# Optimization experiments

Hardware: AMD Instinct MI355X
Metric: run time of the kernel (lower is better)

Reference implementation:

```python
import jax, jax.numpy as jnp
import numpy as np

KLD_SCALE = 10.0
COMMITMENT_COST = 0.1


def setup_inputs() -> dict:
    key = jax.random.key(0)
    k1, k2 = jax.random.split(key)
    z = jax.random.normal(k1, (32, 2048, 64), dtype=jnp.float32)
    codebook = jax.random.normal(k2, (1024, 64), dtype=jnp.float32)
    return {"z": z, "codebook": codebook}


def reference(z, codebook):
    B, N, D = z.shape
    z_e = z.reshape(B * N, D)                          # (M, D)
    # squared euclidean distance: ||z||^2 - 2 z.E^T + ||E||^2
    dist = (
        jnp.sum(z_e * z_e, axis=1, keepdims=True)
        - 2.0 * (z_e @ codebook.T)
        + jnp.sum(codebook * codebook, axis=1)[None, :]
    )                                                  # (M, K)
    ind = jnp.argmin(dist, axis=1)                     # (M,)
    z_q = codebook[ind]                                # (M, D) gather
    latent_loss = (
        COMMITMENT_COST * jnp.mean((jax.lax.stop_gradient(z_q) - z_e) ** 2)
        + jnp.mean((z_q - jax.lax.stop_gradient(z_e)) ** 2)
    ) * KLD_SCALE
    # straight-through estimator
    z_q_st = z_e + jax.lax.stop_gradient(z_q - z_e)
    return z_q_st.reshape(B, N, D), latent_loss
```

## Files before the change

kernel.cpp:

```cpp
#include <hip/hip_runtime.h>
#include <hip/hip_bf16.h>
#include <float.h>

#define DIMS 64
#define KC 1024
#define M_TOTAL 65536
#define TAU 4e-3f

typedef __attribute__((ext_vector_type(8))) short bf16x8;
typedef __attribute__((ext_vector_type(4))) float f32x4;

#define SE_OFF   0
#define CTL_OFF  1024
#define PART_OFF 2048
#define PBH_OFF  4096
#define PBL_OFF  36864
#define IDX_OFF  69632
#define WL_OFF   135168

__device__ inline short f2bf(float x) {
  union { __hip_bfloat16 h; short s; } u;
  u.h = __float2bfloat16(x);
  return u.s;
}
__device__ inline float bf2f(short x) {
  union { short s; __hip_bfloat16 h; } u;
  u.s = x;
  return __bfloat162float(u.h);
}

__device__ inline void gload_lds16(const void* g, void* l) {
  __builtin_amdgcn_global_load_lds(
      (const __attribute__((address_space(1))) void*)g,
      (__attribute__((address_space(3))) void*)l, 16, 0, 0);
}

__global__ __launch_bounds__(256) void k_prep(const float* __restrict__ cb,
                                              float* __restrict__ se,
                                              unsigned int* __restrict__ ctl,
                                              unsigned short* __restrict__ pbh,
                                              unsigned short* __restrict__ pbl) {
  const int tid = blockIdx.x * 256 + threadIdx.x;
  if (tid < 4) ctl[tid] = 0;
  const int l = tid & 63;
  const int s = (tid >> 6) & 1;
  const int tt = tid >> 7;
  const int code = tt * 16 + (l & 15);
  const int k = s * 32 + (l >> 4) * 8;
  const float* p = cb + (size_t)code * DIMS + k;
  float v[8];
  ((float4*)v)[0] = ((const float4*)p)[0];
  ((float4*)v)[1] = ((const float4*)p)[1];
  bf16x8 h, lo;
#pragma unroll
  for (int j = 0; j < 8; ++j) {
    short hj = f2bf(v[j]);
    h[j] = hj;
    lo[j] = f2bf(v[j] - bf2f(hj));
  }
  *(bf16x8*)(pbh + (size_t)tid * 8) = h;
  *(bf16x8*)(pbl + (size_t)tid * 8) = lo;

  if (tid < KC) {
    const float4* q = (const float4*)(cb + (size_t)tid * DIMS);
    float a0 = 0.f, a1 = 0.f, a2 = 0.f, a3 = 0.f;
#pragma unroll
    for (int i = 0; i < DIMS / 4; ++i) {
      float4 u = q[i];
      a0 = fmaf(u.x, u.x, a0);
      a1 = fmaf(u.y, u.y, a1);
      a2 = fmaf(u.z, u.z, a2);
      a3 = fmaf(u.w, u.w, a3);
    }
    se[tid] = (a0 + a1) + (a2 + a3);
  }
}

__global__ __launch_bounds__(256, 4) void k_dist(const float* __restrict__ z,
                                                 const unsigned short* __restrict__ pbh,
                                                 const unsigned short* __restrict__ pbl,
                                                 const float* __restrict__ se,
                                                 int* __restrict__ idxo,
                                                 int* __restrict__ wl,
                                                 unsigned int* __restrict__ ctl) {
  __shared__ bf16x8 sB[2][2][256];
  const int l = threadIdx.x & 63;
  const int w = threadIdx.x >> 6;
  const int r0 = blockIdx.x * 64 + w * 16;
  const int col = l & 15;
  const int g = l >> 4;

  bf16x8 ah[2], al[2];
  {
    const float* zp = z + (size_t)(r0 + col) * DIMS + g * 8;
#pragma unroll
    for (int ks = 0; ks < 2; ++ks) {
      float v[8];
      ((float4*)v)[0] = ((const float4*)(zp + ks * 32))[0];
      ((float4*)v)[1] = ((const float4*)(zp + ks * 32))[1];
#pragma unroll
      for (int j = 0; j < 8; ++j) {
        short hj = f2bf(v[j]);
        ah[ks][j] = hj;
        al[ks][j] = f2bf(v[j] - bf2f(hj));
      }
    }
  }

  float m1[4] = {FLT_MAX, FLT_MAX, FLT_MAX, FLT_MAX};
  float m2[4] = {FLT_MAX, FLT_MAX, FLT_MAX, FLT_MAX};
  int bt[4] = {0, 0, 0, 0};

  {
    const int f = w * 64 + l;
    gload_lds16(pbh + (size_t)f * 8, &sB[0][0][w * 64]);
    gload_lds16(pbl + (size_t)f * 8, &sB[0][1][w * 64]);
  }
  __syncthreads();

  int cur = 0;
  for (int c = 0; c < 32; ++c) {
    if (c + 1 < 32) {
      const size_t f = (size_t)(c + 1) * 256 + w * 64 + l;
      gload_lds16(pbh + f * 8, &sB[cur ^ 1][0][w * 64]);
      gload_lds16(pbl + f * 8, &sB[cur ^ 1][1][w * 64]);
    }
#pragma unroll
    for (int tt = 0; tt < 2; ++tt) {
      const int t = c * 2 + tt;
      bf16x8 bh0 = sB[cur][0][tt * 128 + l];
      bf16x8 bh1 = sB[cur][0][tt * 128 + 64 + l];
      bf16x8 bl0 = sB[cur][1][tt * 128 + l];
      bf16x8 bl1 = sB[cur][1][tt * 128 + 64 + l];
      const float sec = se[t * 16 + col];
      f32x4 acc = {0.f, 0.f, 0.f, 0.f};
      acc = __builtin_amdgcn_mfma_f32_16x16x32_bf16(ah[0], bh0, acc, 0, 0, 0);
      acc = __builtin_amdgcn_mfma_f32_16x16x32_bf16(ah[1], bh1, acc, 0, 0, 0);
      acc = __builtin_amdgcn_mfma_f32_16x16x32_bf16(ah[0], bl0, acc, 0, 0, 0);
      acc = __builtin_amdgcn_mfma_f32_16x16x32_bf16(ah[1], bl1, acc, 0, 0, 0);
      acc = __builtin_amdgcn_mfma_f32_16x16x32_bf16(al[0], bh0, acc, 0, 0, 0);
      acc = __builtin_amdgcn_mfma_f32_16x16x32_bf16(al[1], bh1, acc, 0, 0, 0);
#pragma unroll
      for (int j = 0; j < 4; ++j) {
        float d = fmaf(-2.f, acc[j], sec);
        float nm2 = __builtin_amdgcn_fmed3f(d, m1[j], m2[j]);
        bool lt = d < m1[j];
        m1[j] = lt ? d : m1[j];
        bt[j] = lt ? t : bt[j];
        m2[j] = nm2;
      }
    }
    __syncthreads();
    cur ^= 1;
  }

#pragma unroll
  for (int j = 0; j < 4; ++j) {
    float m1j = m1[j], m2j = m2[j];
    int ij = bt[j] * 16 + col;
    for (int msk = 1; msk <= 8; msk <<= 1) {
      float o1 = __shfl_xor(m1j, msk);
      float o2 = __shfl_xor(m2j, msk);
      int oi = __shfl_xor(ij, msk);
      bool take = (o1 < m1j) || (o1 == m1j && oi < ij);
      float hi = take ? m1j : o1;
      m2j = fminf(fminf(m2j, o2), hi);
      m1j = take ? o1 : m1j;
      ij = take ? oi : ij;
    }
    if (col == 0) {
      const int row = r0 + g * 4 + j;
      idxo[row] = ij;
      if (m2j - m1j < TAU) {
        int p = atomicAdd((int*)ctl, 1);
        wl[p] = row;
      }
    }
  }
}

__global__ __launch_bounds__(256) void k_refine(const float* __restrict__ z,
                                                const float* __restrict__ cb,
                                                const int* __restrict__ wl,
                                                const unsigned int* __restrict__ ctl,
                                                int* __restrict__ idxo) {
  __shared__ float zz[64];
  __shared__ double sd[256];
  __shared__ int si[256];
  const int t = threadIdx.x;
  const int n = (int)ctl[0];
  for (int wi = blockIdx.x; wi < n; wi += 1024) {
    const int row = wl[wi];
    if (t < 16) ((float4*)zz)[t] = ((const float4*)(z + (size_t)row * DIMS))[t];
    __syncthreads();
    const int c0 = t * 4;
    double accd[4] = {0.0, 0.0, 0.0, 0.0};
    for (int ch = 0; ch < 4; ++ch) {
      float zr[16];
#pragma unroll
      for (int q = 0; q < 4; ++q) ((float4*)zr)[q] = ((float4*)zz)[ch * 4 + q];
#pragma unroll
      for (int cc = 0; cc < 4; ++cc) {
        const float* e = cb + (size_t)(c0 + cc) * DIMS + ch * 16;
#pragma unroll
        for (int q = 0; q < 16; ++q) {
          double df = (double)zr[q] - (double)e[q];
          accd[cc] = fma(df, df, accd[cc]);
        }
      }
    }
    double best = 1e300;
    int bi = 0;
#pragma unroll
    for (int cc = 0; cc < 4; ++cc)
      if (accd[cc] < best) { best = accd[cc]; bi = c0 + cc; }
    sd[t] = best;
    si[t] = bi;
    __syncthreads();
    for (int off = 128; off > 0; off >>= 1) {
      if (t < off) {
        double ob = sd[t + off];
        int oi = si[t + off];
        if (ob < sd[t] || (ob == sd[t] && oi < si[t])) { sd[t] = ob; si[t] = oi; }
      }
      __syncthreads();
    }
    if (t == 0) idxo[row] = si[0];
    __syncthreads();
  }
}

__global__ __launch_bounds__(256) void k_out(const float* __restrict__ z,
                                             const float* __restrict__ cb,
                                             const int* __restrict__ idxi,
                                             float* __restrict__ out,
                                             float* __restrict__ partials) {
  const int tid = blockIdx.x * 256 + threadIdx.x;
  const int row = tid >> 2;
  const int q = tid & 3;
  const int code = idxi[row];
  const float4* zp = (const float4*)(z + (size_t)row * DIMS + q * 16);
  const float4* ep = (const float4*)(cb + (size_t)code * DIMS + q * 16);
  float4* op = (float4*)(out + (size_t)row * DIMS + q * 16);
  float sse = 0.f;
#pragma unroll
  for (int i = 0; i < 4; ++i) {
    float4 v = zp[i], e = ep[i];
    float dx = e.x - v.x, dy = e.y - v.y, dz = e.z - v.z, dw = e.w - v.w;
    sse = fmaf(dx, dx, sse);
    sse = fmaf(dy, dy, sse);
    sse = fmaf(dz, dz, sse);
    sse = fmaf(dw, dw, sse);
    float4 o;
    o.x = v.x + dx;
    o.y = v.y + dy;
    o.z = v.z + dz;
    o.w = v.w + dw;
    op[i] = o;
  }
  __shared__ float sh[256];
  sh[threadIdx.x] = sse;
  __syncthreads();
  for (int off = 128; off > 0; off >>= 1) {
    if (threadIdx.x < off) sh[threadIdx.x] += sh[threadIdx.x + off];
    __syncthreads();
  }
  if (threadIdx.x == 0) partials[blockIdx.x] = sh[0];
}

__global__ __launch_bounds__(256) void k_loss(const float* __restrict__ partials,
                                              float* __restrict__ out) {
  __shared__ float sh[256];
  const int t = threadIdx.x;
  sh[t] = partials[t] + partials[t + 256] + partials[t + 512] + partials[t + 768];
  __syncthreads();
  for (int off = 128; off > 0; off >>= 1) {
    if (t < off) sh[t] += sh[t + off];
    __syncthreads();
  }
  if (t == 0) {
    out[(size_t)M_TOTAL * DIMS] = sh[0] * (11.0f / (float)((size_t)M_TOTAL * DIMS));
  }
}

extern "C" void kernel_launch(void* const* d_in, const int* in_sizes, int n_in,
                              void* d_out, int out_size, void* d_ws, size_t ws_size,
                              hipStream_t stream) {
  const float* z = (const float*)d_in[0];
  const float* cb = (const float*)d_in[1];
  float* out = (float*)d_out;
  float* ws = (float*)d_ws;

  float* se = ws + SE_OFF;
  unsigned int* ctl = (unsigned int*)(ws + CTL_OFF);
  float* partials = ws + PART_OFF;
  unsigned short* pbh = (unsigned short*)(ws + PBH_OFF);
  unsigned short* pbl = (unsigned short*)(ws + PBL_OFF);
  int* idx = (int*)(ws + IDX_OFF);
  int* wl = (int*)(ws + WL_OFF);

  k_prep<<<32, 256, 0, stream>>>(cb, se, ctl, pbh, pbl);
  k_dist<<<M_TOTAL / 64, 256, 0, stream>>>(z, pbh, pbl, se, idx, wl, ctl);
  k_refine<<<1024, 256, 0, stream>>>(z, cb, wl, ctl, idx);
  k_out<<<M_TOTAL / 64, 256, 0, stream>>>(z, cb, idx, out, partials);
  k_loss<<<1, 256, 0, stream>>>(partials, out);
}
```

Measured before the change: 61.39 us.

## Split codebook scan across two blocks per row tile and merge top-2 results

The distance kernel now splits the 1024-entry codebook into two halves, so each row tile is handled by two blocks that each scan 512 codes, doubling grid size. It also raises the launch-bounds occupancy hint to 8 blocks. Per-half best/second-best distances and indices go to workspace, and a new merge kernel combines them and builds the ambiguous-row worklist. This targets low occupancy or parallelism in k_dist, at the cost of recomputing the z bf16 split per half, extra global traffic, and another kernel launch.

```diff
diff --git a/kernel.cpp b/kernel.cpp
--- a/kernel.cpp
+++ b/kernel.cpp
@@ -15,8 +15,10 @@
 #define PART_OFF 2048
 #define PBH_OFF  4096
 #define PBL_OFF  36864
-#define IDX_OFF  69632
-#define WL_OFF   135168
+#define M1_OFF   69632
+#define M2_OFF   200704
+#define IDX_OFF  331776
+#define WL_OFF   462848
 
 __device__ inline short f2bf(float x) {
   union { __hip_bfloat16 h; short s; } u;
@@ -76,17 +78,19 @@
   }
 }
 
-__global__ __launch_bounds__(256, 4) void k_dist(const float* __restrict__ z,
+__global__ __launch_bounds__(256, 8) void k_dist(const float* __restrict__ z,
                                                  const unsigned short* __restrict__ pbh,
                                                  const unsigned short* __restrict__ pbl,
                                                  const float* __restrict__ se,
-                                                 int* __restrict__ idxo,
-                                                 int* __restrict__ wl,
-                                                 unsigned int* __restrict__ ctl) {
+                                                 float* __restrict__ m1o,
+                                                 float* __restrict__ m2o,
+                                                 int* __restrict__ idxo) {
   __shared__ bf16x8 sB[2][2][256];
   const int l = threadIdx.x & 63;
   const int w = threadIdx.x >> 6;
-  const int r0 = blockIdx.x * 64 + w * 16;
+  const int split = blockIdx.x & 1;
+  const int rb = blockIdx.x >> 1;
+  const int r0 = rb * 64 + w * 16;
   const int col = l & 15;
   const int g = l >> 4;
 
@@ -111,23 +115,24 @@
   float m2[4] = {FLT_MAX, FLT_MAX, FLT_MAX, FLT_MAX};
   int bt[4] = {0, 0, 0, 0};
 
+  const int C0 = split * 16;
   {
-    const int f = w * 64 + l;
-    gload_lds16(pbh + (size_t)f * 8, &sB[0][0][w * 64]);
-    gload_lds16(pbl + (size_t)f * 8, &sB[0][1][w * 64]);
+    const size_t f = (size_t)C0 * 256 + w * 64 + l;
+    gload_lds16(pbh + f * 8, &sB[0][0][w * 64]);
+    gload_lds16(pbl + f * 8, &sB[0][1][w * 64]);
   }
   __syncthreads();
 
   int cur = 0;
-  for (int c = 0; c < 32; ++c) {
-    if (c + 1 < 32) {
-      const size_t f = (size_t)(c + 1) * 256 + w * 64 + l;
+  for (int c = 0; c < 16; ++c) {
+    if (c + 1 < 16) {
+      const size_t f = (size_t)(C0 + c + 1) * 256 + w * 64 + l;
       gload_lds16(pbh + f * 8, &sB[cur ^ 1][0][w * 64]);
       gload_lds16(pbl + f * 8, &sB[cur ^ 1][1][w * 64]);
     }
 #pragma unroll
     for (int tt = 0; tt < 2; ++tt) {
-      const int t = c * 2 + tt;
+      const int t = (C0 + c) * 2 + tt;
       bf16x8 bh0 = sB[cur][0][tt * 128 + l];
       bf16x8 bh1 = sB[cur][0][tt * 128 + 64 + l];
       bf16x8 bl0 = sB[cur][1][tt * 128 + l];
@@ -169,13 +174,29 @@
       ij = take ? oi : ij;
     }
     if (col == 0) {
-      const int row = r0 + g * 4 + j;
-      idxo[row] = ij;
-      if (m2j - m1j < TAU) {
-        int p = atomicAdd((int*)ctl, 1);
-        wl[p] = row;
-      }
-    }
+      const int o = split * M_TOTAL + r0 + g * 4 + j;
+      m1o[o] = m1j;
+      m2o[o] = m2j;
+      idxo[o] = ij;
+    }
+  }
+}
+
+__global__ __launch_bounds__(256) void k_merge(const float* __restrict__ m1s,
+                                               const float* __restrict__ m2s,
+                                               int* __restrict__ idxs,
+                                               int* __restrict__ wl,
+                                               unsigned int* __restrict__ ctl) {
+  const int row = blockIdx.x * 256 + threadIdx.x;
+  const float a1 = m1s[row], b1 = m1s[M_TOTAL + row];
+  const float a2 = m2s[row], b2 = m2s[M_TOTAL + row];
+  const int ia = idxs[row], ib = idxs[M_TOTAL + row];
+  const float m1 = fminf(a1, b1);
+  const float m2 = fminf(fmaxf(a1, b1), fminf(a2, b2));
+  idxs[row] = (b1 < a1) ? ib : ia;
+  if (m2 - m1 < TAU) {
+    int p = atomicAdd((int*)ctl, 1);
+    wl[p] = row;
   }
 }
 
@@ -296,11 +317,14 @@
   float* partials = ws + PART_OFF;
   unsigned short* pbh = (unsigned short*)(ws + PBH_OFF);
   unsigned short* pbl = (unsigned short*)(ws + PBL_OFF);
+  float* m1s = ws + M1_OFF;
+  float* m2s = ws + M2_OFF;
   int* idx = (int*)(ws + IDX_OFF);
   int* wl = (int*)(ws + WL_OFF);
 
   k_prep<<<32, 256, 0, stream>>>(cb, se, ctl, pbh, pbl);
-  k_dist<<<M_TOTAL / 64, 256, 0, stream>>>(z, pbh, pbl, se, idx, wl, ctl);
+  k_dist<<<(M_TOTAL / 64) * 2, 256, 0, stream>>>(z, pbh, pbl, se, m1s, m2s, idx);
+  k_merge<<<M_TOTAL / 256, 256, 0, stream>>>(m1s, m2s, idx, wl, ctl);
   k_refine<<<1024, 256, 0, stream>>>(z, cb, wl, ctl, idx);
   k_out<<<M_TOTAL / 64, 256, 0, stream>>>(z, cb, idx, out, partials);
   k_loss<<<1, 256, 0, stream>>>(partials, out);
```

New measurement: 80.81 us. 1.32x slower.

## Fuse output gather and per-row SSE into distance kernel, refine patches rows

Applied to the files above, without the earlier changes.

Moves the output gather, straight-through write and squared-error computation into the distance kernel's epilogue, using the block's argmin indices held in shared memory. Per-row SSE values go to a workspace array. The refine kernel now rewrites the output row and its SSE for ambiguous rows, and a single 1024-thread kernel reduces all row SSEs. This removes one full kernel launch and the round trip of the index array through global memory. The cost is more work in k_dist's epilogue, a 256KB per-row SSE array, and an output write that happens twice for refined rows.

```diff
diff --git a/kernel.cpp b/kernel.cpp
--- a/kernel.cpp
+++ b/kernel.cpp
@@ -12,11 +12,10 @@
 
 #define SE_OFF   0
 #define CTL_OFF  1024
-#define PART_OFF 2048
 #define PBH_OFF  4096
 #define PBL_OFF  36864
-#define IDX_OFF  69632
-#define WL_OFF   135168
+#define WL_OFF   69632
+#define SROW_OFF 135168
 
 __device__ inline short f2bf(float x) {
   union { __hip_bfloat16 h; short s; } u;
@@ -80,10 +79,13 @@
                                                  const unsigned short* __restrict__ pbh,
                                                  const unsigned short* __restrict__ pbl,
                                                  const float* __restrict__ se,
-                                                 int* __restrict__ idxo,
+                                                 const float* __restrict__ cb,
+                                                 float* __restrict__ out,
+                                                 float* __restrict__ srow,
                                                  int* __restrict__ wl,
                                                  unsigned int* __restrict__ ctl) {
   __shared__ bf16x8 sB[2][2][256];
+  __shared__ int s_idx[64];
   const int l = threadIdx.x & 63;
   const int w = threadIdx.x >> 6;
   const int r0 = blockIdx.x * 64 + w * 16;
@@ -169,83 +171,26 @@
       ij = take ? oi : ij;
     }
     if (col == 0) {
-      const int row = r0 + g * 4 + j;
-      idxo[row] = ij;
+      s_idx[w * 16 + g * 4 + j] = ij;
       if (m2j - m1j < TAU) {
         int p = atomicAdd((int*)ctl, 1);
-        wl[p] = row;
-      }
-    }
-  }
-}
-
-__global__ __launch_bounds__(256) void k_refine(const float* __restrict__ z,
-                                                const float* __restrict__ cb,
-                                                const int* __restrict__ wl,
-                                                const unsigned int* __restrict__ ctl,
-                                                int* __restrict__ idxo) {
-  __shared__ float zz[64];
-  __shared__ double sd[256];
-  __shared__ int si[256];
-  const int t = threadIdx.x;
-  const int n = (int)ctl[0];
-  for (int wi = blockIdx.x; wi < n; wi += 1024) {
-    const int row = wl[wi];
-    if (t < 16) ((float4*)zz)[t] = ((const float4*)(z + (size_t)row * DIMS))[t];
-    __syncthreads();
-    const int c0 = t * 4;
-    double accd[4] = {0.0, 0.0, 0.0, 0.0};
-    for (int ch = 0; ch < 4; ++ch) {
-      float zr[16];
-#pragma unroll
-      for (int q = 0; q < 4; ++q) ((float4*)zr)[q] = ((float4*)zz)[ch * 4 + q];
-#pragma unroll
-      for (int cc = 0; cc < 4; ++cc) {
-        const float* e = cb + (size_t)(c0 + cc) * DIMS + ch * 16;
-#pragma unroll
-        for (int q = 0; q < 16; ++q) {
-          double df = (double)zr[q] - (double)e[q];
-          accd[cc] = fma(df, df, accd[cc]);
-        }
-      }
-    }
-    double best = 1e300;
-    int bi = 0;
-#pragma unroll
-    for (int cc = 0; cc < 4; ++cc)
-      if (accd[cc] < best) { best = accd[cc]; bi = c0 + cc; }
-    sd[t] = best;
-    si[t] = bi;
-    __syncthreads();
-    for (int off = 128; off > 0; off >>= 1) {
-      if (t < off) {
-        double ob = sd[t + off];
-        int oi = si[t + off];
-        if (ob < sd[t] || (ob == sd[t] && oi < si[t])) { sd[t] = ob; si[t] = oi; }
-      }
-      __syncthreads();
-    }
-    if (t == 0) idxo[row] = si[0];
-    __syncthreads();
-  }
-}
-
-__global__ __launch_bounds__(256) void k_out(const float* __restrict__ z,
-                                             const float* __restrict__ cb,
-                                             const int* __restrict__ idxi,
-                                             float* __restrict__ out,
-                                             float* __restrict__ partials) {
-  const int tid = blockIdx.x * 256 + threadIdx.x;
-  const int row = tid >> 2;
-  const int q = tid & 3;
-  const int code = idxi[row];
-  const float4* zp = (const float4*)(z + (size_t)row * DIMS + q * 16);
-  const float4* ep = (const float4*)(cb + (size_t)code * DIMS + q * 16);
+        wl[p] = r0 + g * 4 + j;
+      }
+    }
+  }
+  __syncthreads();
+
+  const int lr = threadIdx.x >> 2;
+  const int q = threadIdx.x & 3;
+  const int row = blockIdx.x * 64 + lr;
+  const int code = s_idx[lr];
+  const float4* zp4 = (const float4*)(z + (size_t)row * DIMS + q * 16);
+  const float4* ep4 = (const float4*)(cb + (size_t)code * DIMS + q * 16);
   float4* op = (float4*)(out + (size_t)row * DIMS + q * 16);
   float sse = 0.f;
 #pragma unroll
   for (int i = 0; i < 4; ++i) {
-    float4 v = zp[i], e = ep[i];
+    float4 v = zp4[i], e = ep4[i];
     float dx = e.x - v.x, dy = e.y - v.y, dz = e.z - v.z, dw = e.w - v.w;
     sse = fmaf(dx, dx, sse);
     sse = fmaf(dy, dy, sse);
@@ -258,23 +203,102 @@
     o.w = v.w + dw;
     op[i] = o;
   }
-  __shared__ float sh[256];
-  sh[threadIdx.x] = sse;
+  sse += __shfl_xor(sse, 1);
+  sse += __shfl_xor(sse, 2);
+  if (q == 0) srow[row] = sse;
+}
+
+__global__ __launch_bounds__(256) void k_refine(const float* __restrict__ z,
+                                                const float* __restrict__ cb,
+                                                const int* __restrict__ wl,
+                                                const unsigned int* __restrict__ ctl,
+                                                float* __restrict__ out,
+                                                float* __restrict__ srow) {
+  __shared__ float zz[64];
+  __shared__ double sd[256];
+  __shared__ int si[256];
+  __shared__ float s_pf[16];
+  const int t = threadIdx.x;
+  const int n = (int)ctl[0];
+  for (int wi = blockIdx.x; wi < n; wi += 1024) {
+    const int row = wl[wi];
+    if (t < 16) ((float4*)zz)[t] = ((const float4*)(z + (size_t)row * DIMS))[t];
+    __syncthreads();
+    const int c0 = t * 4;
+    double accd[4] = {0.0, 0.0, 0.0, 0.0};
+    for (int ch = 0; ch < 4; ++ch) {
+      float zr[16];
+#pragma unroll
+      for (int q = 0; q < 4; ++q) ((float4*)zr)[q] = ((float4*)zz)[ch * 4 + q];
+#pragma unroll
+      for (int cc = 0; cc < 4; ++cc) {
+        const float* e = cb + (size_t)(c0 + cc) * DIMS + ch * 16;
+#pragma unroll
+        for (int q = 0; q < 16; ++q) {
+          double df = (double)zr[q] - (double)e[q];
+          accd[cc] = fma(df, df, accd[cc]);
+        }
+      }
+    }
+    double best = 1e300;
+    int bi = 0;
+#pragma unroll
+    for (int cc = 0; cc < 4; ++cc)
+      if (accd[cc] < best) { best = accd[cc]; bi = c0 + cc; }
+    sd[t] = best;
+    si[t] = bi;
+    __syncthreads();
+    for (int off = 128; off > 0; off >>= 1) {
+      if (t < off) {
+        double ob = sd[t + off];
+        int oi = si[t + off];
+        if (ob < sd[t] || (ob == sd[t] && oi < si[t])) { sd[t] = ob; si[t] = oi; }
+      }
+      __syncthreads();
+    }
+    const int code = si[0];
+    if (t < 16) {
+      float4 v = ((const float4*)zz)[t];
+      float4 e = ((const float4*)(cb + (size_t)code * DIMS))[t];
+      float dx = e.x - v.x, dy = e.y - v.y, dz = e.z - v.z, dw = e.w - v.w;
+      float s4 = dx * dx;
+      s4 = fmaf(dy, dy, s4);
+      s4 = fmaf(dz, dz, s4);
+      s4 = fmaf(dw, dw, s4);
+      s_pf[t] = s4;
+      float4 o;
+      o.x = v.x + dx;
+      o.y = v.y + dy;
+      o.z = v.z + dz;
+      o.w = v.w + dw;
+      ((float4*)(out + (size_t)row * DIMS))[t] = o;
+    }
+    __syncthreads();
+    if (t == 0) {
+      float s = 0.f;
+#pragma unroll
+      for (int i = 0; i < 16; ++i) s += s_pf[i];
+      srow[row] = s;
+    }
+    __syncthreads();
+  }
+}
+
+__global__ __launch_bounds__(1024) void k_loss(const float* __restrict__ srow,
+                                               float* __restrict__ out) {
+  __shared__ float sh[1024];
+  const int t = threadIdx.x;
+  float a0 = 0.f, a1 = 0.f, a2 = 0.f, a3 = 0.f;
+#pragma unroll
+  for (int i = 0; i < 16; ++i) {
+    a0 += srow[t + (4 * i + 0) * 1024];
+    a1 += srow[t + (4 * i + 1) * 1024];
+    a2 += srow[t + (4 * i + 2) * 1024];
+    a3 += srow[t + (4 * i + 3) * 1024];
+  }
+  sh[t] = (a0 + a1) + (a2 + a3);
   __syncthreads();
-  for (int off = 128; off > 0; off >>= 1) {
-    if (threadIdx.x < off) sh[threadIdx.x] += sh[threadIdx.x + off];
-    __syncthreads();
-  }
-  if (threadIdx.x == 0) partials[blockIdx.x] = sh[0];
-}
-
-__global__ __launch_bounds__(256) void k_loss(const float* __restrict__ partials,
-                                              float* __restrict__ out) {
-  __shared__ float sh[256];
-  const int t = threadIdx.x;
-  sh[t] = partials[t] + partials[t + 256] + partials[t + 512] + partials[t + 768];
-  __syncthreads();
-  for (int off = 128; off > 0; off >>= 1) {
+  for (int off = 512; off > 0; off >>= 1) {
     if (t < off) sh[t] += sh[t + off];
     __syncthreads();
   }
@@ -293,15 +317,13 @@
 
   float* se = ws + SE_OFF;
   unsigned int* ctl = (unsigned int*)(ws + CTL_OFF);
-  float* partials = ws + PART_OFF;
   unsigned short* pbh = (unsigned short*)(ws + PBH_OFF);
   unsigned short* pbl = (unsigned short*)(ws + PBL_OFF);
-  int* idx = (int*)(ws + IDX_OFF);
   int* wl = (int*)(ws + WL_OFF);
+  float* srow = ws + SROW_OFF;
 
   k_prep<<<32, 256, 0, stream>>>(cb, se, ctl, pbh, pbl);
-  k_dist<<<M_TOTAL / 64, 256, 0, stream>>>(z, pbh, pbl, se, idx, wl, ctl);
-  k_refine<<<1024, 256, 0, stream>>>(z, cb, wl, ctl, idx);
-  k_out<<<M_TOTAL / 64, 256, 0, stream>>>(z, cb, idx, out, partials);
-  k_loss<<<1, 256, 0, stream>>>(partials, out);
-}
+  k_dist<<<M_TOTAL / 64, 256, 0, stream>>>(z, pbh, pbl, se, cb, out, srow, wl, ctl);
+  k_refine<<<1024, 256, 0, stream>>>(z, cb, wl, ctl, out, srow);
+  k_loss<<<1, 1024, 0, stream>>>(srow, out);
+}
```

New measurement: 62.60 us. No clear change (+2.0%).
